# Kernel tuning notes

Measured on AMD Instinct MI355X. Metric: run time of the kernel, lower is better.

The kernel has to match this reference:

```python
import jax, jax.numpy as jnp
import numpy as np

M_MOL = 8192      # number of molecules
A_ATOMS = 32      # atoms per molecule (uniform ragged groups)
N_FEAT = 128      # schnet n_atom_basis


def setup_inputs() -> dict:
    key = jax.random.key(0)
    sr = jax.random.normal(key, (M_MOL * A_ATOMS, N_FEAT), dtype=jnp.float32)
    # idx_m: sorted molecule index per atom, uniform group sizes
    idx_m = jnp.repeat(jnp.arange(M_MOL, dtype=jnp.int32), A_ATOMS)
    return {"scalar_representation": sr, "idx_m": idx_m}


def reference(scalar_representation, idx_m):
    # maxm = int(idx_m[-1]) + 1 in the torch code; groups are uniform here so
    # torch.split over bincount == a simple reshape into [M, A, F].
    maxm = int(idx_m[-1]) + 1
    n_atoms = scalar_representation.shape[0]
    a = n_atoms // maxm
    sr = scalar_representation.reshape(maxm, a, -1)          # [M, A, F]
    # per-molecule correlation (Gram) matrix: c = sr @ sr.T
    c = jnp.einsum('maf,mbf->mab', sr, sr)                    # [M, A, A]
    # eigvalsh returns ascending eigenvalues; torch code takes [0] (smallest)
    eigvals = jnp.linalg.eigvalsh(c)                          # [M, A]
    return eigvals[:, 0]                                      # [M]
```

## Files before the change

kernel.cpp:

```cpp
#include <hip/hip_runtime.h>
#include <hip/hip_bf16.h>

#define DEVINL __device__ __forceinline__

typedef __attribute__((ext_vector_type(8))) short short8;
typedef __attribute__((ext_vector_type(4))) float f32x4;

DEVINL float rcp_f(float x) { return __builtin_amdgcn_rcpf(x); }

#define LDS_FENCE() __asm__ volatile("" ::: "memory")

template<int CTRL>
DEVINL float dpp_mov(float x) {
  return __int_as_float(__builtin_amdgcn_update_dpp(
      0, __float_as_int(x), CTRL, 0xF, 0xF, true));
}
DEVINL float pair_sum(float x) { return x + dpp_mov<0xB1>(x); }

DEVINL short bf_hi(float f, float& rem) {
  unsigned u = __float_as_uint(f);
  unsigned rh = (u + 0x8000u) >> 16;
  rem = f - __uint_as_float(rh << 16);
  return (short)rh;
}
DEVINL short bf_of(float f) {
  return (short)((__float_as_uint(f) + 0x8000u) >> 16);
}
DEVINL void cvt_hilo(float4 fa, float4 fb, short8& h, short8& lo) {
  float rm;
  h[0] = bf_hi(fa.x, rm); lo[0] = bf_of(rm);
  h[1] = bf_hi(fa.y, rm); lo[1] = bf_of(rm);
  h[2] = bf_hi(fa.z, rm); lo[2] = bf_of(rm);
  h[3] = bf_hi(fa.w, rm); lo[3] = bf_of(rm);
  h[4] = bf_hi(fb.x, rm); lo[4] = bf_of(rm);
  h[5] = bf_hi(fb.y, rm); lo[5] = bf_of(rm);
  h[6] = bf_hi(fb.z, rm); lo[6] = bf_of(rm);
  h[7] = bf_hi(fb.w, rm); lo[7] = bf_of(rm);
}
DEVINL f32x4 mfma_bf16(short8 a, short8 b, f32x4 c) {
  return __builtin_amdgcn_mfma_f32_16x16x32_bf16(a, b, c, 0, 0, 0);
}

__global__ __launch_bounds__(256) void gram_kernel(
    const float* __restrict__ A, float* __restrict__ W, int M) {
  const int lane = threadIdx.x & 63;
  const int wave = threadIdx.x >> 6;
  const int q    = lane >> 4;
  const int t    = lane & 15;
  const int a    = lane >> 5;
  const int l    = lane & 31;
  const int molbase = blockIdx.x * 8 + wave * 2;
  if (molbase >= M) return;

  __shared__ float ldsT[4][2][32 * 36 + 8];

  #pragma unroll 1
  for (int g = 0; g < 2; ++g) {
    const float* Am = A + (size_t)(molbase + g) * (32 * 128);
    f32x4 acc00 = {0.f, 0.f, 0.f, 0.f}, acc01 = {0.f, 0.f, 0.f, 0.f};
    f32x4 acc10 = {0.f, 0.f, 0.f, 0.f}, acc11 = {0.f, 0.f, 0.f, 0.f};
    #pragma unroll
    for (int c = 0; c < 4; ++c) {
      const float* pr0 = Am + t * 128        + 32 * c + 8 * q;
      const float* pr1 = Am + (t + 16) * 128 + 32 * c + 8 * q;
      float4 fa0 = *(const float4*)(pr0);
      float4 fb0 = *(const float4*)(pr0 + 4);
      float4 fa1 = *(const float4*)(pr1);
      float4 fb1 = *(const float4*)(pr1 + 4);
      short8 h0, l0, h1, l1;
      cvt_hilo(fa0, fb0, h0, l0);
      cvt_hilo(fa1, fb1, h1, l1);
      acc00 = mfma_bf16(h0, h0, acc00); acc00 = mfma_bf16(h0, l0, acc00); acc00 = mfma_bf16(l0, h0, acc00);
      acc01 = mfma_bf16(h0, h1, acc01); acc01 = mfma_bf16(h0, l1, acc01); acc01 = mfma_bf16(l0, h1, acc01);
      acc10 = mfma_bf16(h1, h0, acc10); acc10 = mfma_bf16(h1, l0, acc10); acc10 = mfma_bf16(l1, h0, acc10);
      acc11 = mfma_bf16(h1, h1, acc11); acc11 = mfma_bf16(h1, l1, acc11); acc11 = mfma_bf16(l1, h1, acc11);
    }
    float* tg = &ldsT[wave][g][0];
    #pragma unroll
    for (int reg = 0; reg < 4; ++reg) {
      tg[(4 * q + reg) * 36 + t]           = acc00[reg];
      tg[(4 * q + reg) * 36 + 16 + t]      = acc01[reg];
      tg[(16 + 4 * q + reg) * 36 + t]      = acc10[reg];
      tg[(16 + 4 * q + reg) * 36 + 16 + t] = acc11[reg];
    }
  }
  LDS_FENCE();

  const float* tq = &ldsT[wave][a][0];
  float* Wm = W + (size_t)(molbase + a) * 1024;
  #pragma unroll
  for (int c = 0; c < 8; ++c) {
    float4 x = *(const float4*)(tq + l * 36 + 4 * c);
    *(float4*)(Wm + (c * 32 + l) * 4) = x;
  }
}

template<int K>
DEVINL void house_step(float (&r)[16], int row, int h,
                       float* vbuf, float* pbuf, float* de) {
  constexpr int HK = K >> 4, EK = K & 15;
  constexpr int HP = (K + 1) >> 4, PE = (K + 1) & 15;
  constexpr int PC = PE >> 2, PEE = PE & 3;

  float xm = (row > K) ? r[EK] : 0.0f;
  if (h == HK) vbuf[row] = xm;
  LDS_FENCE();

  float4 vc[4];
  #pragma unroll
  for (int j = 0; j < 4; ++j) vc[j] = *(const float4*)(vbuf + 16 * h + 4 * j);
  float x_me = vbuf[row];
  float x0   = vbuf[K + 1];

  float n0 = 0.f, n1 = 0.f;
  #pragma unroll
  for (int j = 0; j < 4; ++j) {
    n0 = fmaf(vc[j].x, vc[j].x, n0); n1 = fmaf(vc[j].y, vc[j].y, n1);
    n0 = fmaf(vc[j].z, vc[j].z, n0); n1 = fmaf(vc[j].w, vc[j].w, n1);
  }
  float nn = pair_sum(n0 + n1);

  float alpha = -copysignf(sqrtf(nn), x0);
  float denom = nn - alpha * x0;
  float beta  = (denom > 1e-20f) ? rcp_f(denom) : 0.0f;
  float v_me  = x_me - ((row == K + 1) ? alpha : 0.0f);

  if (h == HP) {
    if constexpr (PEE == 0)      vc[PC].x -= alpha;
    else if constexpr (PEE == 1) vc[PC].y -= alpha;
    else if constexpr (PEE == 2) vc[PC].z -= alpha;
    else                         vc[PC].w -= alpha;
  }

  float a0 = 0.f, a1 = 0.f;
  #pragma unroll
  for (int j = 0; j < 4; ++j) {
    a0 = fmaf(r[4 * j + 0], vc[j].x, a0); a1 = fmaf(r[4 * j + 1], vc[j].y, a1);
    a0 = fmaf(r[4 * j + 2], vc[j].z, a0); a1 = fmaf(r[4 * j + 3], vc[j].w, a1);
  }
  float p_me = pair_sum(a0 + a1);
  if (h == 0) pbuf[row] = p_me;
  LDS_FENCE();

  float bv = beta * v_me;
  float bp = (row > K) ? beta * p_me : 0.0f;

  float g0 = 0.f, g1 = 0.f;
  #pragma unroll
  for (int j = 0; j < 4; ++j) {
    float4 pcx = *(const float4*)(pbuf + 16 * h + 4 * j);
    g0 = fmaf(vc[j].x, pcx.x, g0); g1 = fmaf(vc[j].y, pcx.y, g1);
    g0 = fmaf(vc[j].z, pcx.z, g0); g1 = fmaf(vc[j].w, pcx.w, g1);
    r[4 * j + 0] -= bv * pcx.x + bp * vc[j].x;
    r[4 * j + 1] -= bv * pcx.y + bp * vc[j].y;
    r[4 * j + 2] -= bv * pcx.z + bp * vc[j].z;
    r[4 * j + 3] -= bv * pcx.w + bp * vc[j].w;
  }
  float G  = pair_sum(g0 + g1);
  float tv = (beta * beta * G) * v_me;

  #pragma unroll
  for (int j = 0; j < 4; ++j) {
    r[4 * j + 0] = fmaf(tv, vc[j].x, r[4 * j + 0]);
    r[4 * j + 1] = fmaf(tv, vc[j].y, r[4 * j + 1]);
    r[4 * j + 2] = fmaf(tv, vc[j].z, r[4 * j + 2]);
    r[4 * j + 3] = fmaf(tv, vc[j].w, r[4 * j + 3]);
  }

  if (row == K && h == HK) { de[K] = r[EK]; de[32 + K] = alpha; }
}

template<int K>
DEVINL void house_all(float (&r)[16], int row, int h,
                      float* vbuf, float* pbuf, float* de) {
  house_step<K>(r, row, h, vbuf, pbuf, de);
  if constexpr (K < 30) house_all<K + 1>(r, row, h, vbuf, pbuf, de);
}

__global__ __launch_bounds__(256) void house_kernel(
    const float* __restrict__ W, float* __restrict__ DE, int M) {
  const int lane = threadIdx.x & 63;
  const int wave = threadIdx.x >> 6;
  const int row  = lane >> 1;
  const int h    = lane & 1;
  const int mol  = blockIdx.x * 4 + wave;
  if (mol >= M) return;

  __shared__ float sc[4][72];
  float* vbuf = &sc[wave][0];
  float* pbuf = &sc[wave][36];

  const float* Wm = W + (size_t)mol * 1024;
  float r[16];
  #pragma unroll
  for (int j = 0; j < 4; ++j) {
    float4 x = *(const float4*)(Wm + ((4 * h + j) * 32 + row) * 4);
    r[4 * j + 0] = x.x; r[4 * j + 1] = x.y;
    r[4 * j + 2] = x.z; r[4 * j + 3] = x.w;
  }

  float* de = DE + (size_t)mol * 64;
  house_all<0>(r, row, h, vbuf, pbuf, de);
  if (row == 31 && h == 1) { de[31] = r[15]; de[63] = 0.0f; }
}

__global__ __launch_bounds__(256) void sturm_kernel(
    const float* __restrict__ DE, float* __restrict__ out, int M) {
  const int lane = threadIdx.x & 63;
  const int wave = threadIdx.x >> 6;
  const int a = lane >> 5, l = lane & 31;
  const int mol = blockIdx.x * 8 + wave * 2 + a;
  if (mol >= M) return;

  const float* dm = DE + (size_t)mol * 64;
  float vd[32], ve[32];
  #pragma unroll
  for (int c = 0; c < 8; ++c) {
    float4 dc = *(const float4*)(dm + 4 * c);
    float4 ec = *(const float4*)(dm + 32 + 4 * c);
    vd[4 * c + 0] = dc.x; vd[4 * c + 1] = dc.y;
    vd[4 * c + 2] = dc.z; vd[4 * c + 3] = dc.w;
    ve[4 * c + 0] = ec.x; ve[4 * c + 1] = ec.y;
    ve[4 * c + 2] = ec.z; ve[4 * c + 3] = ec.w;
  }
  float glo = vd[0] - fabsf(ve[0]);
  float ghi = vd[0] + fabsf(ve[0]);
  #pragma unroll
  for (int i = 1; i < 32; ++i) {
    float rad = fabsf(ve[i]) + fabsf(ve[i - 1]);
    glo = fminf(glo, vd[i] - rad);
    ghi = fmaxf(ghi, vd[i] + rad);
  }
  float lo = fmaxf(glo - 1e-3f, 0.0f);
  float hi = ghi + 1e-3f;

  #pragma unroll
  for (int i = 0; i < 32; ++i) ve[i] *= ve[i];

  #pragma unroll
  for (int rr = 0; rr < 3; ++rr) {
    float stp = (hi - lo) * (1.0f / 33.0f);
    float sig = fmaf(stp, (float)(l + 1), lo);
    float qq = vd[0] - sig;
    int cnt = (qq < 0.0f) ? 1 : 0;
    #pragma unroll
    for (int i = 1; i < 32; ++i) {
      float qs = (fabsf(qq) < 1e-12f) ? ((qq < 0.0f) ? -1e-12f : 1e-12f) : qq;
      qq = (vd[i] - sig) - ve[i - 1] * rcp_f(qs);
      cnt += (qq < 0.0f) ? 1 : 0;
    }
    unsigned long long m64 = __ballot(cnt >= 1);
    unsigned hm = (unsigned)(m64 >> (a * 32));
    int b = (hm == 0u) ? 32 : (__ffs(hm) - 1);
    float nhi = (b == 32) ? hi : fmaf(stp, (float)(b + 1), lo);
    lo = fmaf(stp, (float)b, lo);
    hi = nhi;
  }

  if (l == 0) out[mol] = 0.5f * (lo + hi);
}

extern "C" void kernel_launch(void* const* d_in, const int* in_sizes, int n_in,
                              void* d_out, int out_size, void* d_ws, size_t ws_size,
                              hipStream_t stream) {
  const float* A = (const float*)d_in[0];
  float* out = (float*)d_out;
  int n_atoms = in_sizes[1];
  int M = n_atoms / 32;
  float* W  = (float*)d_ws;
  float* DE = W + (size_t)M * 1024;
  hipLaunchKernelGGL(gram_kernel,  dim3(M / 8), dim3(256), 0, stream, A, W, M);
  hipLaunchKernelGGL(house_kernel, dim3(M / 4), dim3(256), 0, stream, W, DE, M);
  hipLaunchKernelGGL(sturm_kernel, dim3(M / 8), dim3(256), 0, stream, DE, out, M);
}
```

Baseline: 253.5 us.

## Fuse Gram, Householder tridiagonalization and Sturm bisection into one kernel

```diff
diff --git a/kernel.cpp b/kernel.cpp
--- a/kernel.cpp
+++ b/kernel.cpp
@@ -41,22 +41,104 @@
   return __builtin_amdgcn_mfma_f32_16x16x32_bf16(a, b, c, 0, 0, 0);
 }
 
-__global__ __launch_bounds__(256) void gram_kernel(
-    const float* __restrict__ A, float* __restrict__ W, int M) {
+template<int K>
+DEVINL void house_step(float (&r)[16], int row, int h,
+                       float* vbuf, float* pbuf, float* de) {
+  constexpr int HK = K >> 4, EK = K & 15;
+  constexpr int HP = (K + 1) >> 4, PE = (K + 1) & 15;
+  constexpr int PC = PE >> 2, PEE = PE & 3;
+
+  float xm = (row > K) ? r[EK] : 0.0f;
+  if (h == HK) vbuf[row] = xm;
+  LDS_FENCE();
+
+  float4 vc[4];
+  #pragma unroll
+  for (int j = 0; j < 4; ++j) vc[j] = *(const float4*)(vbuf + 16 * h + 4 * j);
+  float x_me = vbuf[row];
+  float x0   = vbuf[K + 1];
+
+  float n0 = 0.f, n1 = 0.f;
+  #pragma unroll
+  for (int j = 0; j < 4; ++j) {
+    n0 = fmaf(vc[j].x, vc[j].x, n0); n1 = fmaf(vc[j].y, vc[j].y, n1);
+    n0 = fmaf(vc[j].z, vc[j].z, n0); n1 = fmaf(vc[j].w, vc[j].w, n1);
+  }
+  float nn = pair_sum(n0 + n1);
+
+  float alpha = -copysignf(sqrtf(nn), x0);
+  float denom = nn - alpha * x0;
+  float beta  = (denom > 1e-20f) ? rcp_f(denom) : 0.0f;
+  float v_me  = x_me - ((row == K + 1) ? alpha : 0.0f);
+
+  if (h == HP) {
+    if constexpr (PEE == 0)      vc[PC].x -= alpha;
+    else if constexpr (PEE == 1) vc[PC].y -= alpha;
+    else if constexpr (PEE == 2) vc[PC].z -= alpha;
+    else                         vc[PC].w -= alpha;
+  }
+
+  float a0 = 0.f, a1 = 0.f;
+  #pragma unroll
+  for (int j = 0; j < 4; ++j) {
+    a0 = fmaf(r[4 * j + 0], vc[j].x, a0); a1 = fmaf(r[4 * j + 1], vc[j].y, a1);
+    a0 = fmaf(r[4 * j + 2], vc[j].z, a0); a1 = fmaf(r[4 * j + 3], vc[j].w, a1);
+  }
+  float p_me = pair_sum(a0 + a1);
+  if (h == 0) pbuf[row] = p_me;
+  LDS_FENCE();
+
+  float bv = beta * v_me;
+  float bp = (row > K) ? beta * p_me : 0.0f;
+
+  float g0 = 0.f, g1 = 0.f;
+  #pragma unroll
+  for (int j = 0; j < 4; ++j) {
+    float4 pcx = *(const float4*)(pbuf + 16 * h + 4 * j);
+    g0 = fmaf(vc[j].x, pcx.x, g0); g1 = fmaf(vc[j].y, pcx.y, g1);
+    g0 = fmaf(vc[j].z, pcx.z, g0); g1 = fmaf(vc[j].w, pcx.w, g1);
+    r[4 * j + 0] -= bv * pcx.x + bp * vc[j].x;
+    r[4 * j + 1] -= bv * pcx.y + bp * vc[j].y;
+    r[4 * j + 2] -= bv * pcx.z + bp * vc[j].z;
+    r[4 * j + 3] -= bv * pcx.w + bp * vc[j].w;
+  }
+  float G  = pair_sum(g0 + g1);
+  float tv = (beta * beta * G) * v_me;
+
+  #pragma unroll
+  for (int j = 0; j < 4; ++j) {
+    r[4 * j + 0] = fmaf(tv, vc[j].x, r[4 * j + 0]);
+    r[4 * j + 1] = fmaf(tv, vc[j].y, r[4 * j + 1]);
+    r[4 * j + 2] = fmaf(tv, vc[j].z, r[4 * j + 2]);
+    r[4 * j + 3] = fmaf(tv, vc[j].w, r[4 * j + 3]);
+  }
+
+  if (row == K && h == HK) { de[K] = r[EK]; de[32 + K] = alpha; }
+}
+
+template<int K>
+DEVINL void house_all(float (&r)[16], int row, int h,
+                      float* vbuf, float* pbuf, float* de) {
+  house_step<K>(r, row, h, vbuf, pbuf, de);
+  if constexpr (K < 30) house_all<K + 1>(r, row, h, vbuf, pbuf, de);
+}
+
+__global__ __launch_bounds__(256) void Correlation_85134841741354_kernel(
+    const float* __restrict__ A, float* __restrict__ out, int M) {
   const int lane = threadIdx.x & 63;
   const int wave = threadIdx.x >> 6;
   const int q    = lane >> 4;
   const int t    = lane & 15;
-  const int a    = lane >> 5;
-  const int l    = lane & 31;
-  const int molbase = blockIdx.x * 8 + wave * 2;
-  if (molbase >= M) return;
-
-  __shared__ float ldsT[4][2][32 * 36 + 8];
-
-  #pragma unroll 1
-  for (int g = 0; g < 2; ++g) {
-    const float* Am = A + (size_t)(molbase + g) * (32 * 128);
+  const int row  = lane >> 1;
+  const int h    = lane & 1;
+  const int mol  = blockIdx.x * 4 + wave;
+  if (mol >= M) return;
+
+  __shared__ float ldsT[4][32 * 36 + 8];
+  float* tq = &ldsT[wave][0];
+
+  {
+    const float* Am = A + (size_t)mol * (32 * 128);
     f32x4 acc00 = {0.f, 0.f, 0.f, 0.f}, acc01 = {0.f, 0.f, 0.f, 0.f};
     f32x4 acc10 = {0.f, 0.f, 0.f, 0.f}, acc11 = {0.f, 0.f, 0.f, 0.f};
     #pragma unroll
@@ -75,149 +157,38 @@
       acc10 = mfma_bf16(h1, h0, acc10); acc10 = mfma_bf16(h1, l0, acc10); acc10 = mfma_bf16(l1, h0, acc10);
       acc11 = mfma_bf16(h1, h1, acc11); acc11 = mfma_bf16(h1, l1, acc11); acc11 = mfma_bf16(l1, h1, acc11);
     }
-    float* tg = &ldsT[wave][g][0];
     #pragma unroll
     for (int reg = 0; reg < 4; ++reg) {
-      tg[(4 * q + reg) * 36 + t]           = acc00[reg];
-      tg[(4 * q + reg) * 36 + 16 + t]      = acc01[reg];
-      tg[(16 + 4 * q + reg) * 36 + t]      = acc10[reg];
-      tg[(16 + 4 * q + reg) * 36 + 16 + t] = acc11[reg];
+      tq[(4 * q + reg) * 36 + t]           = acc00[reg];
+      tq[(4 * q + reg) * 36 + 16 + t]      = acc01[reg];
+      tq[(16 + 4 * q + reg) * 36 + t]      = acc10[reg];
+      tq[(16 + 4 * q + reg) * 36 + 16 + t] = acc11[reg];
     }
   }
   LDS_FENCE();
 
-  const float* tq = &ldsT[wave][a][0];
-  float* Wm = W + (size_t)(molbase + a) * 1024;
-  #pragma unroll
-  for (int c = 0; c < 8; ++c) {
-    float4 x = *(const float4*)(tq + l * 36 + 4 * c);
-    *(float4*)(Wm + (c * 32 + l) * 4) = x;
-  }
-}
-
-template<int K>
-DEVINL void house_step(float (&r)[16], int row, int h,
-                       float* vbuf, float* pbuf, float* de) {
-  constexpr int HK = K >> 4, EK = K & 15;
-  constexpr int HP = (K + 1) >> 4, PE = (K + 1) & 15;
-  constexpr int PC = PE >> 2, PEE = PE & 3;
-
-  float xm = (row > K) ? r[EK] : 0.0f;
-  if (h == HK) vbuf[row] = xm;
-  LDS_FENCE();
-
-  float4 vc[4];
-  #pragma unroll
-  for (int j = 0; j < 4; ++j) vc[j] = *(const float4*)(vbuf + 16 * h + 4 * j);
-  float x_me = vbuf[row];
-  float x0   = vbuf[K + 1];
-
-  float n0 = 0.f, n1 = 0.f;
-  #pragma unroll
-  for (int j = 0; j < 4; ++j) {
-    n0 = fmaf(vc[j].x, vc[j].x, n0); n1 = fmaf(vc[j].y, vc[j].y, n1);
-    n0 = fmaf(vc[j].z, vc[j].z, n0); n1 = fmaf(vc[j].w, vc[j].w, n1);
-  }
-  float nn = pair_sum(n0 + n1);
-
-  float alpha = -copysignf(sqrtf(nn), x0);
-  float denom = nn - alpha * x0;
-  float beta  = (denom > 1e-20f) ? rcp_f(denom) : 0.0f;
-  float v_me  = x_me - ((row == K + 1) ? alpha : 0.0f);
-
-  if (h == HP) {
-    if constexpr (PEE == 0)      vc[PC].x -= alpha;
-    else if constexpr (PEE == 1) vc[PC].y -= alpha;
-    else if constexpr (PEE == 2) vc[PC].z -= alpha;
-    else                         vc[PC].w -= alpha;
-  }
-
-  float a0 = 0.f, a1 = 0.f;
-  #pragma unroll
-  for (int j = 0; j < 4; ++j) {
-    a0 = fmaf(r[4 * j + 0], vc[j].x, a0); a1 = fmaf(r[4 * j + 1], vc[j].y, a1);
-    a0 = fmaf(r[4 * j + 2], vc[j].z, a0); a1 = fmaf(r[4 * j + 3], vc[j].w, a1);
-  }
-  float p_me = pair_sum(a0 + a1);
-  if (h == 0) pbuf[row] = p_me;
-  LDS_FENCE();
-
-  float bv = beta * v_me;
-  float bp = (row > K) ? beta * p_me : 0.0f;
-
-  float g0 = 0.f, g1 = 0.f;
-  #pragma unroll
-  for (int j = 0; j < 4; ++j) {
-    float4 pcx = *(const float4*)(pbuf + 16 * h + 4 * j);
-    g0 = fmaf(vc[j].x, pcx.x, g0); g1 = fmaf(vc[j].y, pcx.y, g1);
-    g0 = fmaf(vc[j].z, pcx.z, g0); g1 = fmaf(vc[j].w, pcx.w, g1);
-    r[4 * j + 0] -= bv * pcx.x + bp * vc[j].x;
-    r[4 * j + 1] -= bv * pcx.y + bp * vc[j].y;
-    r[4 * j + 2] -= bv * pcx.z + bp * vc[j].z;
-    r[4 * j + 3] -= bv * pcx.w + bp * vc[j].w;
-  }
-  float G  = pair_sum(g0 + g1);
-  float tv = (beta * beta * G) * v_me;
-
-  #pragma unroll
-  for (int j = 0; j < 4; ++j) {
-    r[4 * j + 0] = fmaf(tv, vc[j].x, r[4 * j + 0]);
-    r[4 * j + 1] = fmaf(tv, vc[j].y, r[4 * j + 1]);
-    r[4 * j + 2] = fmaf(tv, vc[j].z, r[4 * j + 2]);
-    r[4 * j + 3] = fmaf(tv, vc[j].w, r[4 * j + 3]);
-  }
-
-  if (row == K && h == HK) { de[K] = r[EK]; de[32 + K] = alpha; }
-}
-
-template<int K>
-DEVINL void house_all(float (&r)[16], int row, int h,
-                      float* vbuf, float* pbuf, float* de) {
-  house_step<K>(r, row, h, vbuf, pbuf, de);
-  if constexpr (K < 30) house_all<K + 1>(r, row, h, vbuf, pbuf, de);
-}
-
-__global__ __launch_bounds__(256) void house_kernel(
-    const float* __restrict__ W, float* __restrict__ DE, int M) {
-  const int lane = threadIdx.x & 63;
-  const int wave = threadIdx.x >> 6;
-  const int row  = lane >> 1;
-  const int h    = lane & 1;
-  const int mol  = blockIdx.x * 4 + wave;
-  if (mol >= M) return;
-
-  __shared__ float sc[4][72];
-  float* vbuf = &sc[wave][0];
-  float* pbuf = &sc[wave][36];
-
-  const float* Wm = W + (size_t)mol * 1024;
   float r[16];
   #pragma unroll
   for (int j = 0; j < 4; ++j) {
-    float4 x = *(const float4*)(Wm + ((4 * h + j) * 32 + row) * 4);
+    float4 x = *(const float4*)(tq + row * 36 + 16 * h + 4 * j);
     r[4 * j + 0] = x.x; r[4 * j + 1] = x.y;
     r[4 * j + 2] = x.z; r[4 * j + 3] = x.w;
   }
-
-  float* de = DE + (size_t)mol * 64;
+  LDS_FENCE();
+
+  float* vbuf = tq;
+  float* pbuf = tq + 40;
+  float* de   = tq + 80;
+
   house_all<0>(r, row, h, vbuf, pbuf, de);
   if (row == 31 && h == 1) { de[31] = r[15]; de[63] = 0.0f; }
-}
-
-__global__ __launch_bounds__(256) void sturm_kernel(
-    const float* __restrict__ DE, float* __restrict__ out, int M) {
-  const int lane = threadIdx.x & 63;
-  const int wave = threadIdx.x >> 6;
-  const int a = lane >> 5, l = lane & 31;
-  const int mol = blockIdx.x * 8 + wave * 2 + a;
-  if (mol >= M) return;
-
-  const float* dm = DE + (size_t)mol * 64;
+  LDS_FENCE();
+
   float vd[32], ve[32];
   #pragma unroll
   for (int c = 0; c < 8; ++c) {
-    float4 dc = *(const float4*)(dm + 4 * c);
-    float4 ec = *(const float4*)(dm + 32 + 4 * c);
+    float4 dc = *(const float4*)(de + 4 * c);
+    float4 ec = *(const float4*)(de + 32 + 4 * c);
     vd[4 * c + 0] = dc.x; vd[4 * c + 1] = dc.y;
     vd[4 * c + 2] = dc.z; vd[4 * c + 3] = dc.w;
     ve[4 * c + 0] = ec.x; ve[4 * c + 1] = ec.y;
@@ -239,8 +210,8 @@
 
   #pragma unroll
   for (int rr = 0; rr < 3; ++rr) {
-    float stp = (hi - lo) * (1.0f / 33.0f);
-    float sig = fmaf(stp, (float)(l + 1), lo);
+    float stp = (hi - lo) * (1.0f / 65.0f);
+    float sig = fmaf(stp, (float)(lane + 1), lo);
     float qq = vd[0] - sig;
     int cnt = (qq < 0.0f) ? 1 : 0;
     #pragma unroll
@@ -250,14 +221,13 @@
       cnt += (qq < 0.0f) ? 1 : 0;
     }
     unsigned long long m64 = __ballot(cnt >= 1);
-    unsigned hm = (unsigned)(m64 >> (a * 32));
-    int b = (hm == 0u) ? 32 : (__ffs(hm) - 1);
-    float nhi = (b == 32) ? hi : fmaf(stp, (float)(b + 1), lo);
+    int b = (m64 == 0ull) ? 64 : (__ffsll((unsigned long long)m64) - 1);
+    float nhi = (b == 64) ? hi : fmaf(stp, (float)(b + 1), lo);
     lo = fmaf(stp, (float)b, lo);
     hi = nhi;
   }
 
-  if (l == 0) out[mol] = 0.5f * (lo + hi);
+  if (lane == 0) out[mol] = 0.5f * (lo + hi);
 }
 
 extern "C" void kernel_launch(void* const* d_in, const int* in_sizes, int n_in,
@@ -267,9 +237,7 @@
   float* out = (float*)d_out;
   int n_atoms = in_sizes[1];
   int M = n_atoms / 32;
-  float* W  = (float*)d_ws;
-  float* DE = W + (size_t)M * 1024;
-  hipLaunchKernelGGL(gram_kernel,  dim3(M / 8), dim3(256), 0, stream, A, W, M);
-  hipLaunchKernelGGL(house_kernel, dim3(M / 4), dim3(256), 0, stream, W, DE, M);
-  hipLaunchKernelGGL(sturm_kernel, dim3(M / 8), dim3(256), 0, stream, DE, out, M);
-}
+  int blocks = (M + 3) / 4;
+  hipLaunchKernelGGL(Correlation_85134841741354_kernel,
+                     dim3(blocks), dim3(256), 0, stream, A, out, M);
+}
```

New measurement: 228.3 us. 9.9% less time.
